# Kernel tuning notes

Measured on AMD Instinct MI355X. Metric: run time of the kernel, lower is better.

Reference implementation:

```python
import jax, jax.numpy as jnp
import numpy as np

H = 768


def lstm_cell(x, h, c, Wih, Whh, b):
    # PyTorch LSTMCell gate order: i, f, g, o
    gates = x @ Wih.T + h @ Whh.T + b
    i, f, g, o = jnp.split(gates, 4, axis=-1)
    c = jax.nn.sigmoid(f) * c + jax.nn.sigmoid(i) * jnp.tanh(g)
    h = jax.nn.sigmoid(o) * jnp.tanh(c)
    return h, c


def run_lstm(x, Wih, Whh, b, reverse):
    B = x.shape[0]
    Hd = Whh.shape[1]
    def step(carry, xt):
        h, c = lstm_cell(xt, carry[0], carry[1], Wih, Whh, b)
        return (h, c), h
    init = (jnp.zeros((B, Hd), x.dtype), jnp.zeros((B, Hd), x.dtype))
    _, hs = jax.lax.scan(step, init, jnp.swapaxes(x, 0, 1), reverse=reverse)
    return jnp.swapaxes(hs, 0, 1)


def _forward(hidden_state, golds, lstm_Wih_f, lstm_Whh_f, lstm_b_f,
             lstm_Wih_b, lstm_Whh_b, lstm_b_b, subw_Wih, subw_Whh, subw_b,
             word_Wih, word_Whh, word_b, cls_W, cls_b):
    B, T, _ = hidden_state.shape
    dt = hidden_state.dtype
    out_f = run_lstm(hidden_state, lstm_Wih_f, lstm_Whh_f, lstm_b_f, False)
    out_b = run_lstm(hidden_state, lstm_Wih_b, lstm_Whh_b, lstm_b_b, True)
    lstm_out = jnp.concatenate([out_f, out_b], -1)  # [B, T, 2H]

    subw_map = jnp.array([1, 2, 2], dtype=jnp.int32)
    word_map = jnp.array([0, 1, 1], dtype=jnp.int32)
    bidx = jnp.arange(B)
    S1, S2 = 2 * T + 2, T + 1
    carry0 = (jnp.zeros((S1, B, H), dt), jnp.zeros((S1, B, H), dt), jnp.zeros((B,), jnp.int32),
              jnp.zeros((S2, B, H), dt), jnp.zeros((S2, B, H), dt), jnp.zeros((B,), jnp.int32))
    xs = (jnp.swapaxes(lstm_out[:, :T - 1], 0, 1),  # features for subword cell at step idx-1
          jnp.swapaxes(lstm_out[:, 1:T], 0, 1),     # features concatenated into cls at step idx
          golds[:, 1:T].T.astype(jnp.int32))

    def step(carry, x):
        sh, sc, spos, wh, wc, wpos = carry
        x_prev, x_cur, g = x
        # subword stack-LSTM: read top-of-stack state, push new state at pos+1
        h1, c1 = lstm_cell(x_prev, sh[spos, bidx], sc[spos, bidx], subw_Wih, subw_Whh, subw_b)
        sh = sh.at[spos + 1, bidx].set(h1)
        sc = sc.at[spos + 1, bidx].set(c1)
        subword = jnp.concatenate([h1, c1], -1)  # [B, 2H] input to word stack-LSTM
        # word stack-LSTM
        h2, c2 = lstm_cell(subword, wh[wpos, bidx], wc[wpos, bidx], word_Wih, word_Whh, word_b)
        wh = wh.at[wpos + 1, bidx].set(h2)
        wc = wc.at[wpos + 1, bidx].set(c2)
        out = jnp.concatenate([h2, x_cur], -1) @ cls_W.T + cls_b  # [B, 2]
        # training path: ops from gold actions
        sop = subw_map[g]
        wop = word_map[g]
        spos = jnp.where(sop == 1, spos + 1, 0)      # APP: push; SEP: clear subword stack
        wpos = jnp.where(wop == 1, wpos + 1, wpos)   # SEP: push word; APP: hold
        return (sh, sc, spos, wh, wc, wpos), out

    _, outs = jax.lax.scan(step, carry0, xs)  # [T-1, B, 2]
    pred0 = jnp.broadcast_to(jnp.asarray([-1.0, 1.0], dt), (1, B, 2))
    return jnp.swapaxes(jnp.concatenate([pred0, outs], 0), 0, 1)  # [B, T, 2]


def setup_inputs() -> dict:
    key = jax.random.key(0)
    ks = jax.random.split(key, 12)
    B, T = 64, 256
    s = 0.02
    W = lambda k, shape: jax.random.normal(k, shape, jnp.float32) * s
    return {
        "hidden_state": jax.random.normal(ks[0], (B, T, H), jnp.float32),
        "golds": jax.random.randint(ks[1], (B, T), 0, 2),
        "lstm_Wih_f": W(ks[2], (4 * H, H)), "lstm_Whh_f": W(ks[3], (4 * H, H)), "lstm_b_f": jnp.zeros((4 * H,), jnp.float32),
        "lstm_Wih_b": W(ks[4], (4 * H, H)), "lstm_Whh_b": W(ks[5], (4 * H, H)), "lstm_b_b": jnp.zeros((4 * H,), jnp.float32),
        "subw_Wih": W(ks[6], (4 * H, 2 * H)), "subw_Whh": W(ks[7], (4 * H, H)), "subw_b": jnp.zeros((4 * H,), jnp.float32),
        "word_Wih": W(ks[8], (4 * H, 2 * H)), "word_Whh": W(ks[9], (4 * H, H)), "word_b": jnp.zeros((4 * H,), jnp.float32),
        "cls_W": W(ks[10], (2, 3 * H)), "cls_b": jnp.zeros((2,), jnp.float32),
    }


def reference(hidden_state, golds, lstm_Wih_f, lstm_Whh_f, lstm_b_f,
              lstm_Wih_b, lstm_Whh_b, lstm_b_b, subw_Wih, subw_Whh, subw_b,
              word_Wih, word_Whh, word_b, cls_W, cls_b):
    return _forward(hidden_state, golds, lstm_Wih_f, lstm_Whh_f, lstm_b_f,
                    lstm_Wih_b, lstm_Whh_b, lstm_b_b, subw_Wih, subw_Whh, subw_b,
                    word_Wih, word_Whh, word_b, cls_W, cls_b)
```

## Files before the change

### kernel.cpp

```cpp
#include <hip/hip_runtime.h>
#include <hip/hip_bf16.h>

typedef __attribute__((ext_vector_type(8))) short bf16x8;
typedef __attribute__((ext_vector_type(4))) float f32x4;
typedef __attribute__((ext_vector_type(4))) unsigned u32x4;

#define HD   768
#define NB   64
#define NT   256
#define NGATE 3072
#define FPAD 32

__device__ __forceinline__ float fast_sig(float x) { return 1.f / (1.f + __expf(-x)); }
__device__ __forceinline__ float fast_tanh(float x) {
  float t = __expf(-2.f * fabsf(x));
  float r = (1.f - t) / (1.f + t);
  return x < 0.f ? -r : r;
}
__device__ __forceinline__ float bf2f(unsigned short u) {
  union { unsigned i; float f; } v; v.i = ((unsigned)u) << 16; return v.f;
}
__device__ __forceinline__ unsigned short f2bfu(float f) {
  union { __hip_bfloat16 b; unsigned short u; } c;
  c.b = __float2bfloat16(f);
  return c.u;
}
__device__ __forceinline__ unsigned pack2(float a, float b) {
  return (unsigned)f2bfu(a) | ((unsigned)f2bfu(b) << 16);
}

__device__ __forceinline__ int aload(int* p) {
  return __hip_atomic_load(p, __ATOMIC_RELAXED, __HIP_MEMORY_SCOPE_AGENT);
}
__device__ __forceinline__ void ustore(unsigned* p, unsigned v) {
  __hip_atomic_store(p, v, __ATOMIC_RELAXED, __HIP_MEMORY_SCOPE_AGENT);
}
__device__ __forceinline__ u32x4 cload16(const char* p) {
  u32x4 r;
  asm volatile("global_load_dwordx4 %0, %1, off sc0 sc1"
               : "=v"(r) : "v"(p) : "memory");
  return r;
}

__device__ __forceinline__ void arrive_flag(int* f) {
  asm volatile("s_waitcnt vmcnt(0)" ::: "memory");
  __syncthreads();
  if (threadIdx.x == 0)
    __hip_atomic_fetch_add(f, 1, __ATOMIC_RELAXED, __HIP_MEMORY_SCOPE_AGENT);
}

__device__ __forceinline__ void wait2(int* fa, int ta, int* fb, int tb) {
  int tid = threadIdx.x;
  int* p = nullptr; int tgt = 0;
  if (tid < 96)                            { p = fa + tid * FPAD;         tgt = ta; }
  else if (fb && tid >= 128 && tid < 224)  { p = fb + (tid - 128) * FPAD; tgt = tb; }
  if (p && tgt > 0) {
    int guard = 0;
    while (aload(p) < tgt) {
      __builtin_amdgcn_s_sleep(1);
      if (++guard > (1 << 17)) break;
    }
  }
  __syncthreads();
}

__device__ __forceinline__ int frag_dw(int b, int j) {
  return (((((j >> 5) * 4 + (b >> 4)) * 4 + ((j >> 3) & 3)) * 16 + (b & 15)) * 4)
         + ((j & 7) >> 1);
}

__device__ __forceinline__ void load_W_lds(unsigned short* Wl,
                                           const __hip_bfloat16* Wg,
                                           int n_base, int K)
{
  int chunksPerRow = (K * 2) / 16;
  int total = 32 * chunksPerRow;
  for (int idx = threadIdx.x; idx < total; idx += 256) {
    int r  = idx / chunksPerRow;
    int cb = (idx % chunksPerRow) * 16;
    bf16x8 v = *(const bf16x8*)((const char*)(Wg + (long)(n_base + r) * K) + cb);
    *(bf16x8*)((char*)Wl + (long)r * (K * 2) + (cb ^ ((r & 7) << 4))) = v;
  }
}

template<int CF>
__device__ __forceinline__ void mfma_frag_range(
    const char* Fbase, int l, int w,
    const char* w0, const char* w1, int xr, int kk, int kbase,
    f32x4& acc0, f32x4& acc1)
{
  const char* fp = Fbase + (size_t)(w * 64 + l) * 16;
  u32x4 st[2][12];
  #pragma unroll
  for (int i = 0; i < 12; ++i)
    st[0][i] = cload16(fp + (size_t)i * 4096);
  #pragma unroll
  for (int c = 0; c < CF / 12; ++c) {
    if (c + 1 < CF / 12) {
      #pragma unroll
      for (int i = 0; i < 12; ++i)
        st[(c + 1) & 1][i] = cload16(fp + (size_t)((c + 1) * 12 + i) * 4096);
      asm volatile("s_waitcnt vmcnt(12)" ::: "memory");
    } else {
      asm volatile("s_waitcnt vmcnt(0)" ::: "memory");
    }
    __builtin_amdgcn_sched_barrier(0);
    #pragma unroll
    for (int i = 0; i < 12; ++i) {
      int it = kbase + c * 12 + i;
      int o = ((it * 32 + kk) * 2) ^ xr;
      bf16x8 av = __builtin_bit_cast(bf16x8, st[c & 1][i]);
      bf16x8 bv0 = *(const bf16x8*)(w0 + o);
      bf16x8 bv1 = *(const bf16x8*)(w1 + o);
      acc0 = __builtin_amdgcn_mfma_f32_16x16x32_bf16(av, bv0, acc0, 0, 0, 0);
      acc1 = __builtin_amdgcn_mfma_f32_16x16x32_bf16(av, bv1, acc1, 0, 0, 0);
    }
  }
}

__device__ __forceinline__ void mfma_cached_range(
    const __hip_bfloat16* a0p, int C0,
    const char* w0, const char* w1, int xr, int kk,
    f32x4& acc0, f32x4& acc1)
{
  #pragma unroll 4
  for (int it = 0; it < C0; ++it) {
    bf16x8 av = *(const bf16x8*)(a0p + it * 32 + kk);
    int o = ((it * 32 + kk) * 2) ^ xr;
    bf16x8 bv0 = *(const bf16x8*)(w0 + o);
    bf16x8 bv1 = *(const bf16x8*)(w1 + o);
    acc0 = __builtin_amdgcn_mfma_f32_16x16x32_bf16(av, bv0, acc0, 0, 0, 0);
    acc1 = __builtin_amdgcn_mfma_f32_16x16x32_bf16(av, bv1, acc1, 0, 0, 0);
  }
}

__global__ void cvt_bf16_kernel(const float* __restrict__ src,
                                __hip_bfloat16* __restrict__ dst, long n)
{
  long i = (long)blockIdx.x * blockDim.x + threadIdx.x;
  long stride = (long)gridDim.x * blockDim.x;
  for (; i < n; i += stride) dst[i] = __float2bfloat16(src[i]);
}

__global__ void pack_w_kernel(const float* __restrict__ Wih,
                              const float* __restrict__ Whh,
                              __hip_bfloat16* __restrict__ dst, int Kih)
{
  int K = Kih + HD;
  long total = (long)NGATE * K;
  long stride = (long)gridDim.x * blockDim.x;
  for (long idx = (long)blockIdx.x * blockDim.x + threadIdx.x; idx < total; idx += stride) {
    int np = (int)(idx / K), k = (int)(idx % K);
    int j = np >> 2, g = np & 3;
    int n = g * HD + j;
    float v = (k < Kih) ? Wih[(long)n * Kih + k] : Whh[(long)n * HD + (k - Kih)];
    dst[idx] = __float2bfloat16(v);
  }
}

__global__ void fill_sentinel(float* out, int n, float v)
{
  int i = blockIdx.x * blockDim.x + threadIdx.x;
  if (i < n) out[i] = v;
}

__global__ __launch_bounds__(256, 1) void bilstm_persist(
    const __hip_bfloat16* __restrict__ X16,
    const __hip_bfloat16* __restrict__ WF,
    const __hip_bfloat16* __restrict__ WB,
    const float* __restrict__ bF, const float* __restrict__ bB,
    unsigned* __restrict__ H16u,
    __hip_bfloat16* __restrict__ L16,
    int* __restrict__ flags)
{
  __shared__ unsigned short Wl[32 * 1536];
  __shared__ float gl[64][33];
  int blk = blockIdx.x, dir = blk / 96, nt = blk % 96;
  load_W_lds(Wl, dir ? WB : WF, nt * 32, 1536);
  const float* bias = dir ? bB : bF;
  int* myflags = flags + dir * 96 * FPAD;
  int tid = threadIdx.x;
  unsigned* L16u = (unsigned*)L16;

  int w = tid >> 6, l = tid & 63, lr = l & 15, lh = l >> 4;
  const char* w0 = (const char*)Wl + lr * 3072;
  const char* w1 = (const char*)Wl + (16 + lr) * 3072;
  int xr = (lr & 7) << 4;
  int kk = 8 * lh;
  int bA = 16 * w + lr;

  int e0 = tid * 2;
  int b = e0 >> 3, jj = e0 & 7;
  int j0 = nt * 8 + jj;
  float bv[2][4];
  #pragma unroll
  for (int u = 0; u < 2; ++u) {
    bv[u][0] = bias[j0 + u];          bv[u][1] = bias[HD + j0 + u];
    bv[u][2] = bias[2 * HD + j0 + u]; bv[u][3] = bias[3 * HD + j0 + u];
  }
  int fdw = frag_dw(b, j0);
  float cst[2] = {0.f, 0.f};
  __syncthreads();

  for (int s = 0; s < NT; ++s) {
    int par = s & 1;
    int t = dir ? (NT - 1 - s) : s;
    if (s > 0) wait2(myflags, s, nullptr, 0);
    f32x4 acc0 = {0.f, 0.f, 0.f, 0.f};
    f32x4 acc1 = {0.f, 0.f, 0.f, 0.f};
    mfma_cached_range(X16 + (long)t * HD + (long)bA * (NT * HD), 24,
                      w0, w1, xr, kk, acc0, acc1);
    mfma_frag_range<24>((const char*)(H16u + (long)(par * 2 + dir) * 24576),
                        l, w, w0, w1, xr, kk, 24, acc0, acc1);
    #pragma unroll
    for (int r = 0; r < 4; ++r) {
      gl[16 * w + 4 * lh + r][lr]      = acc0[r];
      gl[16 * w + 4 * lh + r][16 + lr] = acc1[r];
    }
    __syncthreads();
    float hv[2];
    #pragma unroll
    for (int u = 0; u < 2; ++u) {
      int col = 4 * (jj + u);
      float vi = gl[b][col + 0] + bv[u][0];
      float vf = gl[b][col + 1] + bv[u][1];
      float vg = gl[b][col + 2] + bv[u][2];
      float vo = gl[b][col + 3] + bv[u][3];
      float si = fast_sig(vi), sf = fast_sig(vf), so = fast_sig(vo);
      float tg = fast_tanh(vg);
      float c = sf * cst[u] + si * tg;
      cst[u] = c;
      hv[u] = so * fast_tanh(c);
    }
    unsigned pk = pack2(hv[0], hv[1]);
    ustore(H16u + (long)((par ^ 1) * 2 + dir) * 24576 + fdw, pk);
    L16u[((long)b * NT + t) * 768 + dir * 384 + (j0 >> 1)] = pk;
    if (s < NT - 1) arrive_flag(myflags + nt * FPAD);
  }
}

__global__ __launch_bounds__(256) void clsx_kernel(
    const __hip_bfloat16* __restrict__ L16,
    const float* __restrict__ clsW, const float* __restrict__ clsb,
    float* __restrict__ out)
{
  int t = blockIdx.x;
  int tid = threadIdx.x;
  if (tid >= 128) return;
  int b = tid >> 1, o = tid & 1;
  if (t == 0) {
    out[((long)b * NT) * 2 + o] = o ? 1.f : -1.f;
    return;
  }
  const bf16x8* xp = (const bf16x8*)(L16 + ((long)b * NT + t) * 1536);
  const float* w = clsW + o * 2304 + HD;
  float s = clsb[o];
  for (int k = 0; k < 192; ++k) {
    bf16x8 v = xp[k];
    #pragma unroll
    for (int e = 0; e < 8; ++e)
      s += bf2f((unsigned short)v[e]) * w[k * 8 + e];
  }
  out[((long)b * NT + t) * 2 + o] = s;
}

__global__ __launch_bounds__(256, 1) void stack_persist(
    const __hip_bfloat16* __restrict__ L16,
    const __hip_bfloat16* __restrict__ WS,
    const __hip_bfloat16* __restrict__ WW,
    const float* __restrict__ bS, const float* __restrict__ bW,
    const int* __restrict__ golds,
    const float* __restrict__ clsW,
    unsigned* __restrict__ H1Su,
    unsigned* __restrict__ H2Su,
    unsigned* __restrict__ SUBWu,
    float* __restrict__ out,
    int* __restrict__ flags)
{
  __shared__ unsigned short Wl[32 * 2304];
  __shared__ float gl[64][33];
  int blk = blockIdx.x, role = blk / 96, nt = blk % 96;
  int* flagS = flags + 2 * 96 * FPAD;
  int* flagW = flags + 3 * 96 * FPAD;
  const float* bias = role ? bW : bS;
  load_W_lds(Wl, role ? WW : WS, nt * 32, 2304);
  int tid = threadIdx.x;

  int w = tid >> 6, l = tid & 63, lr = l & 15, lh = l >> 4;
  const char* w0 = (const char*)Wl + lr * 4608;
  const char* w1 = (const char*)Wl + (16 + lr) * 4608;
  int xr = (lr & 7) << 4;
  int kk = 8 * lh;
  int bA = 16 * w + lr;

  int e0 = tid * 2;
  int b = e0 >> 3, jj = e0 & 7;
  int j0 = nt * 8 + jj;
  float bv[2][4];
  #pragma unroll
  for (int u = 0; u < 2; ++u) {
    bv[u][0] = bias[j0 + u];          bv[u][1] = bias[HD + j0 + u];
    bv[u][2] = bias[2 * HD + j0 + u]; bv[u][3] = bias[3 * HD + j0 + u];
  }
  const int* gp = golds + b * NT + 1;
  int fdw_h = frag_dw(b, j0);
  float cst[2] = {0.f, 0.f};
  float hreg[2] = {0.f, 0.f};
  __syncthreads();

  if (role == 0) {
    int fdw_c = frag_dw(b, 768 + j0);
    for (int s = 0; s < NT - 1; ++s) {
      wait2(flagS, s, flagW, s - 3);
      f32x4 acc0 = {0.f, 0.f, 0.f, 0.f};
      f32x4 acc1 = {0.f, 0.f, 0.f, 0.f};
      mfma_cached_range(L16 + (long)s * 1536 + (long)bA * (NT * 1536), 48,
                        w0, w1, xr, kk, acc0, acc1);
      mfma_frag_range<24>((const char*)(H1Su + (long)(s & 1) * 24576),
                          l, w, w0, w1, xr, kk, 48, acc0, acc1);
      #pragma unroll
      for (int r = 0; r < 4; ++r) {
        gl[16 * w + 4 * lh + r][lr]      = acc0[r];
        gl[16 * w + 4 * lh + r][16 + lr] = acc1[r];
      }
      __syncthreads();
      float h1v[2], c1v[2];
      #pragma unroll
      for (int u = 0; u < 2; ++u) {
        int col = 4 * (jj + u);
        float vi = gl[b][col + 0] + bv[u][0];
        float vf = gl[b][col + 1] + bv[u][1];
        float vg = gl[b][col + 2] + bv[u][2];
        float vo = gl[b][col + 3] + bv[u][3];
        float si = fast_sig(vi), sf = fast_sig(vf), so = fast_sig(vo);
        float tg = fast_tanh(vg);
        c1v[u] = sf * cst[u] + si * tg;
        h1v[u] = so * fast_tanh(c1v[u]);
      }
      int g = gp[s];
      bool push = (g == 0);
      unsigned pkh = pack2(h1v[0], h1v[1]);
      unsigned pkc = pack2(c1v[0], c1v[1]);
      unsigned* sb = SUBWu + (long)(s & 3) * 49152;
      ustore(sb + fdw_h, pkh);
      ustore(sb + fdw_c, pkc);
      ustore(H1Su + (long)((s + 1) & 1) * 24576 + fdw_h, push ? pkh : 0u);
      cst[0] = push ? c1v[0] : 0.f;
      cst[1] = push ? c1v[1] : 0.f;
      arrive_flag(flagS + nt * FPAD);
    }
  } else {
    float cw0[2], cw1[2];
    #pragma unroll
    for (int u = 0; u < 2; ++u) { cw0[u] = clsW[j0 + u]; cw1[u] = clsW[2304 + j0 + u]; }
    for (int s = 0; s < NT - 1; ++s) {
      wait2(flagS, s + 1, flagW, s);
      f32x4 acc0 = {0.f, 0.f, 0.f, 0.f};
      f32x4 acc1 = {0.f, 0.f, 0.f, 0.f};
      mfma_frag_range<48>((const char*)(SUBWu + (long)(s & 3) * 49152),
                          l, w, w0, w1, xr, kk, 0, acc0, acc1);
      mfma_frag_range<24>((const char*)(H2Su + (long)(s & 1) * 24576),
                          l, w, w0, w1, xr, kk, 48, acc0, acc1);
      #pragma unroll
      for (int r = 0; r < 4; ++r) {
        gl[16 * w + 4 * lh + r][lr]      = acc0[r];
        gl[16 * w + 4 * lh + r][16 + lr] = acc1[r];
      }
      __syncthreads();
      float p0 = 0.f, p1 = 0.f;
      float h2v[2], c2v[2];
      #pragma unroll
      for (int u = 0; u < 2; ++u) {
        int col = 4 * (jj + u);
        float vi = gl[b][col + 0] + bv[u][0];
        float vf = gl[b][col + 1] + bv[u][1];
        float vg = gl[b][col + 2] + bv[u][2];
        float vo = gl[b][col + 3] + bv[u][3];
        float si = fast_sig(vi), sf = fast_sig(vf), so = fast_sig(vo);
        float tg = fast_tanh(vg);
        c2v[u] = sf * cst[u] + si * tg;
        h2v[u] = so * fast_tanh(c2v[u]);
        p0 += h2v[u] * cw0[u];
        p1 += h2v[u] * cw1[u];
      }
      int g = gp[s];
      bool push = (g >= 1);
      #pragma unroll
      for (int u = 0; u < 2; ++u) {
        cst[u]  = push ? c2v[u] : cst[u];
        hreg[u] = push ? h2v[u] : hreg[u];
      }
      ustore(H2Su + (long)((s + 1) & 1) * 24576 + fdw_h, pack2(hreg[0], hreg[1]));
      p0 += __shfl_down(p0, 1); p1 += __shfl_down(p1, 1);
      p0 += __shfl_down(p0, 2); p1 += __shfl_down(p1, 2);
      if ((tid & 3) == 0) {
        int bb = tid >> 2;
        atomicAdd(&out[((long)bb * NT + s + 1) * 2 + 0], p0);
        atomicAdd(&out[((long)bb * NT + s + 1) * 2 + 1], p1);
      }
      if (s < NT - 2) arrive_flag(flagW + nt * FPAD);
    }
  }
}

extern "C" void kernel_launch(void* const* d_in, const int* in_sizes, int n_in,
                              void* d_out, int out_size, void* d_ws, size_t ws_size,
                              hipStream_t stream)
{
  const float* x     = (const float*)d_in[0];
  const int*   golds = (const int*)d_in[1];
  const float* WihF  = (const float*)d_in[2];
  const float* WhhF  = (const float*)d_in[3];
  const float* bF    = (const float*)d_in[4];
  const float* WihB  = (const float*)d_in[5];
  const float* WhhB  = (const float*)d_in[6];
  const float* bB    = (const float*)d_in[7];
  const float* WihS  = (const float*)d_in[8];
  const float* WhhS  = (const float*)d_in[9];
  const float* bS    = (const float*)d_in[10];
  const float* WihW  = (const float*)d_in[11];
  const float* WhhW  = (const float*)d_in[12];
  const float* bW    = (const float*)d_in[13];
  const float* clsW  = (const float*)d_in[14];
  const float* clsb  = (const float*)d_in[15];
  float* out = (float*)d_out;

  const size_t OFF_X16  = 0;
  const size_t OFF_WF   = 25165824;
  const size_t OFF_WB   = 34603008;
  const size_t OFF_WS   = 44040192;
  const size_t OFF_WW   = 58195968;
  const size_t OFF_L16  = 72351744;
  const size_t OFF_H16  = 122683392;
  const size_t OFF_H1S  = 123076608;
  const size_t OFF_H2S  = 123273216;
  const size_t OFF_SUBW = 123469824;
  const size_t OFF_FLG  = 124256256;
  const size_t WS_NEEDED = 124305408;

  if (ws_size < WS_NEEDED) {
    fill_sentinel<<<(out_size + 255) / 256, 256, 0, stream>>>(out, out_size, 12345.f);
    return;
  }

  char* ws = (char*)d_ws;
  __hip_bfloat16* X16  = (__hip_bfloat16*)(ws + OFF_X16);
  __hip_bfloat16* WF   = (__hip_bfloat16*)(ws + OFF_WF);
  __hip_bfloat16* WB   = (__hip_bfloat16*)(ws + OFF_WB);
  __hip_bfloat16* WSp  = (__hip_bfloat16*)(ws + OFF_WS);
  __hip_bfloat16* WWp  = (__hip_bfloat16*)(ws + OFF_WW);
  __hip_bfloat16* L16  = (__hip_bfloat16*)(ws + OFF_L16);
  unsigned*       H16u = (unsigned*)(ws + OFF_H16);
  unsigned*       H1Su = (unsigned*)(ws + OFF_H1S);
  unsigned*       H2Su = (unsigned*)(ws + OFF_H2S);
  unsigned*       SUBWu= (unsigned*)(ws + OFF_SUBW);
  int*            flags= (int*)(ws + OFF_FLG);

  pack_w_kernel<<<2048, 256, 0, stream>>>(WihF, WhhF, WF, 768);
  pack_w_kernel<<<2048, 256, 0, stream>>>(WihB, WhhB, WB, 768);
  pack_w_kernel<<<2048, 256, 0, stream>>>(WihS, WhhS, WSp, 1536);
  pack_w_kernel<<<2048, 256, 0, stream>>>(WihW, WhhW, WWp, 1536);
  cvt_bf16_kernel<<<2048, 256, 0, stream>>>(x, X16, (long)NB * NT * HD);
  hipMemsetAsync(ws + OFF_H16, 0, WS_NEEDED - OFF_H16, stream);

  bilstm_persist<<<192, 256, 0, stream>>>(X16, WF, WB, bF, bB, H16u, L16, flags);

  clsx_kernel<<<NT, 256, 0, stream>>>(L16, clsW, clsb, out);

  stack_persist<<<192, 256, 0, stream>>>(L16, WSp, WWp, bS, bW, golds, clsW,
                                         H1Su, H2Su, SUBWu, out, flags);
}
```

Baseline: 4.733 ms.

## Overlap input GEMM with flag wait, widen LDS swizzle, fuse setup kernels

```diff
diff --git a/kernel.cpp b/kernel.cpp
--- a/kernel.cpp
+++ b/kernel.cpp
@@ -69,6 +69,10 @@
          + ((j & 7) >> 1);
 }
 
+__device__ __forceinline__ int wswz(int r) {
+  return ((r & 7) << 4) | (((r >> 3) & 3) << 7);
+}
+
 __device__ __forceinline__ void load_W_lds(unsigned short* Wl,
                                            const __hip_bfloat16* Wg,
                                            int n_base, int K)
@@ -79,14 +83,30 @@
     int r  = idx / chunksPerRow;
     int cb = (idx % chunksPerRow) * 16;
     bf16x8 v = *(const bf16x8*)((const char*)(Wg + (long)(n_base + r) * K) + cb);
-    *(bf16x8*)((char*)Wl + (long)r * (K * 2) + (cb ^ ((r & 7) << 4))) = v;
+    *(bf16x8*)((char*)Wl + (long)r * (K * 2) + (cb ^ wswz(r))) = v;
+  }
+}
+
+__device__ __forceinline__ void mfma_cached(
+    const __hip_bfloat16* a0p, int NIT,
+    const char* w0, const char* w1, int xr0, int xr1, int kk,
+    f32x4& acc0, f32x4& acc1)
+{
+  #pragma unroll 4
+  for (int it = 0; it < NIT; ++it) {
+    bf16x8 av = *(const bf16x8*)(a0p + it * 32 + kk);
+    int oo = (it * 32 + kk) * 2;
+    bf16x8 bv0 = *(const bf16x8*)(w0 + (oo ^ xr0));
+    bf16x8 bv1 = *(const bf16x8*)(w1 + (oo ^ xr1));
+    acc0 = __builtin_amdgcn_mfma_f32_16x16x32_bf16(av, bv0, acc0, 0, 0, 0);
+    acc1 = __builtin_amdgcn_mfma_f32_16x16x32_bf16(av, bv1, acc1, 0, 0, 0);
   }
 }
 
 template<int CF>
-__device__ __forceinline__ void mfma_frag_range(
+__device__ __forceinline__ void mfma_frag(
     const char* Fbase, int l, int w,
-    const char* w0, const char* w1, int xr, int kk, int kbase,
+    const char* w0, const char* w1, int xr0, int xr1, int kk, int kbase,
     f32x4& acc0, f32x4& acc1)
 {
   const char* fp = Fbase + (size_t)(w * 64 + l) * 16;
@@ -107,55 +127,49 @@
     __builtin_amdgcn_sched_barrier(0);
     #pragma unroll
     for (int i = 0; i < 12; ++i) {
-      int it = kbase + c * 12 + i;
-      int o = ((it * 32 + kk) * 2) ^ xr;
+      int oo = ((kbase + c * 12 + i) * 32 + kk) * 2;
       bf16x8 av = __builtin_bit_cast(bf16x8, st[c & 1][i]);
-      bf16x8 bv0 = *(const bf16x8*)(w0 + o);
-      bf16x8 bv1 = *(const bf16x8*)(w1 + o);
+      bf16x8 bv0 = *(const bf16x8*)(w0 + (oo ^ xr0));
+      bf16x8 bv1 = *(const bf16x8*)(w1 + (oo ^ xr1));
       acc0 = __builtin_amdgcn_mfma_f32_16x16x32_bf16(av, bv0, acc0, 0, 0, 0);
       acc1 = __builtin_amdgcn_mfma_f32_16x16x32_bf16(av, bv1, acc1, 0, 0, 0);
     }
   }
 }
 
-__device__ __forceinline__ void mfma_cached_range(
-    const __hip_bfloat16* a0p, int C0,
-    const char* w0, const char* w1, int xr, int kk,
-    f32x4& acc0, f32x4& acc1)
-{
-  #pragma unroll 4
-  for (int it = 0; it < C0; ++it) {
-    bf16x8 av = *(const bf16x8*)(a0p + it * 32 + kk);
-    int o = ((it * 32 + kk) * 2) ^ xr;
-    bf16x8 bv0 = *(const bf16x8*)(w0 + o);
-    bf16x8 bv1 = *(const bf16x8*)(w1 + o);
-    acc0 = __builtin_amdgcn_mfma_f32_16x16x32_bf16(av, bv0, acc0, 0, 0, 0);
-    acc1 = __builtin_amdgcn_mfma_f32_16x16x32_bf16(av, bv1, acc1, 0, 0, 0);
-  }
-}
-
-__global__ void cvt_bf16_kernel(const float* __restrict__ src,
-                                __hip_bfloat16* __restrict__ dst, long n)
-{
-  long i = (long)blockIdx.x * blockDim.x + threadIdx.x;
-  long stride = (long)gridDim.x * blockDim.x;
-  for (; i < n; i += stride) dst[i] = __float2bfloat16(src[i]);
-}
-
-__global__ void pack_w_kernel(const float* __restrict__ Wih,
-                              const float* __restrict__ Whh,
-                              __hip_bfloat16* __restrict__ dst, int Kih)
+__device__ __forceinline__ void pack_seg(const float* Wih, const float* Whh,
+                                         __hip_bfloat16* dst, int Kih,
+                                         long id0, long stride)
 {
   int K = Kih + HD;
   long total = (long)NGATE * K;
-  long stride = (long)gridDim.x * blockDim.x;
-  for (long idx = (long)blockIdx.x * blockDim.x + threadIdx.x; idx < total; idx += stride) {
+  for (long idx = id0; idx < total; idx += stride) {
     int np = (int)(idx / K), k = (int)(idx % K);
     int j = np >> 2, g = np & 3;
     int n = g * HD + j;
     float v = (k < Kih) ? Wih[(long)n * Kih + k] : Whh[(long)n * HD + (k - Kih)];
     dst[idx] = __float2bfloat16(v);
   }
+}
+
+__global__ void setup_kernel(
+    const float* __restrict__ x,
+    const float* __restrict__ WihF, const float* __restrict__ WhhF,
+    const float* __restrict__ WihB, const float* __restrict__ WhhB,
+    const float* __restrict__ WihS, const float* __restrict__ WhhS,
+    const float* __restrict__ WihW, const float* __restrict__ WhhW,
+    __hip_bfloat16* __restrict__ X16,
+    __hip_bfloat16* __restrict__ WF, __hip_bfloat16* __restrict__ WB,
+    __hip_bfloat16* __restrict__ WS, __hip_bfloat16* __restrict__ WW)
+{
+  long id0 = (long)blockIdx.x * blockDim.x + threadIdx.x;
+  long stride = (long)gridDim.x * blockDim.x;
+  for (long i = id0; i < (long)NB * NT * HD; i += stride)
+    X16[i] = __float2bfloat16(x[i]);
+  pack_seg(WihF, WhhF, WF, 768, id0, stride);
+  pack_seg(WihB, WhhB, WB, 768, id0, stride);
+  pack_seg(WihS, WhhS, WS, 1536, id0, stride);
+  pack_seg(WihW, WhhW, WW, 1536, id0, stride);
 }
 
 __global__ void fill_sentinel(float* out, int n, float v)
@@ -185,7 +199,7 @@
   int w = tid >> 6, l = tid & 63, lr = l & 15, lh = l >> 4;
   const char* w0 = (const char*)Wl + lr * 3072;
   const char* w1 = (const char*)Wl + (16 + lr) * 3072;
-  int xr = (lr & 7) << 4;
+  int xr0 = wswz(lr), xr1 = wswz(16 + lr);
   int kk = 8 * lh;
   int bA = 16 * w + lr;
 
@@ -205,13 +219,13 @@
   for (int s = 0; s < NT; ++s) {
     int par = s & 1;
     int t = dir ? (NT - 1 - s) : s;
-    if (s > 0) wait2(myflags, s, nullptr, 0);
     f32x4 acc0 = {0.f, 0.f, 0.f, 0.f};
     f32x4 acc1 = {0.f, 0.f, 0.f, 0.f};
-    mfma_cached_range(X16 + (long)t * HD + (long)bA * (NT * HD), 24,
-                      w0, w1, xr, kk, acc0, acc1);
-    mfma_frag_range<24>((const char*)(H16u + (long)(par * 2 + dir) * 24576),
-                        l, w, w0, w1, xr, kk, 24, acc0, acc1);
+    mfma_cached(X16 + (long)t * HD + (long)bA * (NT * HD), 24,
+                w0, w1, xr0, xr1, kk, acc0, acc1);
+    if (s > 0) wait2(myflags, s, nullptr, 0);
+    mfma_frag<24>((const char*)(H16u + (long)(par * 2 + dir) * 24576),
+                  l, w, w0, w1, xr0, xr1, kk, 24, acc0, acc1);
     #pragma unroll
     for (int r = 0; r < 4; ++r) {
       gl[16 * w + 4 * lh + r][lr]      = acc0[r];
@@ -289,7 +303,7 @@
   int w = tid >> 6, l = tid & 63, lr = l & 15, lh = l >> 4;
   const char* w0 = (const char*)Wl + lr * 4608;
   const char* w1 = (const char*)Wl + (16 + lr) * 4608;
-  int xr = (lr & 7) << 4;
+  int xr0 = wswz(lr), xr1 = wswz(16 + lr);
   int kk = 8 * lh;
   int bA = 16 * w + lr;
 
@@ -311,13 +325,13 @@
   if (role == 0) {
     int fdw_c = frag_dw(b, 768 + j0);
     for (int s = 0; s < NT - 1; ++s) {
-      wait2(flagS, s, flagW, s - 3);
       f32x4 acc0 = {0.f, 0.f, 0.f, 0.f};
       f32x4 acc1 = {0.f, 0.f, 0.f, 0.f};
-      mfma_cached_range(L16 + (long)s * 1536 + (long)bA * (NT * 1536), 48,
-                        w0, w1, xr, kk, acc0, acc1);
-      mfma_frag_range<24>((const char*)(H1Su + (long)(s & 1) * 24576),
-                          l, w, w0, w1, xr, kk, 48, acc0, acc1);
+      mfma_cached(L16 + (long)s * 1536 + (long)bA * (NT * 1536), 48,
+                  w0, w1, xr0, xr1, kk, acc0, acc1);
+      wait2(flagS, s, flagW, s - 3);
+      mfma_frag<24>((const char*)(H1Su + (long)(s & 1) * 24576),
+                    l, w, w0, w1, xr0, xr1, kk, 48, acc0, acc1);
       #pragma unroll
       for (int r = 0; r < 4; ++r) {
         gl[16 * w + 4 * lh + r][lr]      = acc0[r];
@@ -354,13 +368,14 @@
     #pragma unroll
     for (int u = 0; u < 2; ++u) { cw0[u] = clsW[j0 + u]; cw1[u] = clsW[2304 + j0 + u]; }
     for (int s = 0; s < NT - 1; ++s) {
-      wait2(flagS, s + 1, flagW, s);
+      wait2(flagW, s, nullptr, 0);
       f32x4 acc0 = {0.f, 0.f, 0.f, 0.f};
       f32x4 acc1 = {0.f, 0.f, 0.f, 0.f};
-      mfma_frag_range<48>((const char*)(SUBWu + (long)(s & 3) * 49152),
-                          l, w, w0, w1, xr, kk, 0, acc0, acc1);
-      mfma_frag_range<24>((const char*)(H2Su + (long)(s & 1) * 24576),
-                          l, w, w0, w1, xr, kk, 48, acc0, acc1);
+      mfma_frag<24>((const char*)(H2Su + (long)(s & 1) * 24576),
+                    l, w, w0, w1, xr0, xr1, kk, 48, acc0, acc1);
+      wait2(flagS, s + 1, nullptr, 0);
+      mfma_frag<48>((const char*)(SUBWu + (long)(s & 3) * 49152),
+                    l, w, w0, w1, xr0, xr1, kk, 0, acc0, acc1);
       #pragma unroll
       for (int r = 0; r < 4; ++r) {
         gl[16 * w + 4 * lh + r][lr]      = acc0[r];
@@ -456,11 +471,9 @@
   unsigned*       SUBWu= (unsigned*)(ws + OFF_SUBW);
   int*            flags= (int*)(ws + OFF_FLG);
 
-  pack_w_kernel<<<2048, 256, 0, stream>>>(WihF, WhhF, WF, 768);
-  pack_w_kernel<<<2048, 256, 0, stream>>>(WihB, WhhB, WB, 768);
-  pack_w_kernel<<<2048, 256, 0, stream>>>(WihS, WhhS, WSp, 1536);
-  pack_w_kernel<<<2048, 256, 0, stream>>>(WihW, WhhW, WWp, 1536);
-  cvt_bf16_kernel<<<2048, 256, 0, stream>>>(x, X16, (long)NB * NT * HD);
+  setup_kernel<<<4096, 256, 0, stream>>>(x, WihF, WhhF, WihB, WhhB,
+                                         WihS, WhhS, WihW, WhhW,
+                                         X16, WF, WB, WSp, WWp);
   hipMemsetAsync(ws + OFF_H16, 0, WS_NEEDED - OFF_H16, stream);
 
   bilstm_persist<<<192, 256, 0, stream>>>(X16, WF, WB, bF, bB, H16u, L16, flags);
```

After: 4.056 ms. -14.3%, faster.
